# Kernel tuning notes

Measured on AMD Instinct MI355X. Metric: run time of the kernel, lower is better.

Reference implementation:

```python
import jax, jax.numpy as jnp
import numpy as np

N_LEVELS = 4
F_DIM = 2
B = 1_000_000
SIZES = [12 * ((2 ** (l - 1)) ** 2 + 2) for l in range(1, N_LEVELS + 1)]  # [36, 72, 216, 792]
MAX_SIZE = max(SIZES)  # 792
NPIX = [12 * (2 ** i) ** 2 for i in range(N_LEVELS)]  # [12, 48, 192, 768]


def setup_inputs() -> dict:
    key = jax.random.key(0)
    ks = jax.random.split(key, 6)
    # learned table, init uniform(-1e-4, 1e-4) as in the torch module
    params = jax.random.uniform(ks[0], (N_LEVELS, MAX_SIZE, F_DIM),
                                minval=-1e-4, maxval=1e-4, dtype=jnp.float32)
    # per-level HEALPix pixel indices, each in [0, npix_level)
    pixel_index = jnp.stack([
        jax.random.randint(jax.random.fold_in(ks[1], i), (B,), 0, NPIX[i], dtype=jnp.int32)
        for i in range(N_LEVELS)])
    neigh = jnp.stack([
        jax.random.randint(jax.random.fold_in(ks[2], i), (8, B), 0, NPIX[i], dtype=jnp.int32)
        for i in range(N_LEVELS)])
    drop = jax.random.uniform(ks[3], (N_LEVELS, 8, B)) < 0.05
    neigh_index = jnp.where(drop, jnp.int32(-1), neigh)
    # latlon in radians: theta in [0, pi], phi in [0, 2*pi)
    u_p = jax.random.uniform(ks[4], (N_LEVELS, B, 2))
    pixel_latlon = jnp.stack([u_p[..., 0] * jnp.pi, u_p[..., 1] * (2 * jnp.pi)], axis=-1).astype(jnp.float32)
    u_n = jax.random.uniform(ks[5], (N_LEVELS, 8 * B, 2))
    neigh_latlon = jnp.stack([u_n[..., 0] * jnp.pi, u_n[..., 1] * (2 * jnp.pi)], axis=-1).astype(jnp.float32)
    return {"params": params, "pixel_latlon": pixel_latlon, "neigh_latlon": neigh_latlon,
            "pixel_index": pixel_index, "neigh_index": neigh_index}


def reference(params, pixel_latlon, neigh_latlon, pixel_index, neigh_index):
    L, _, F = params.shape  # [L, max_size, F]
    Bp = pixel_index.shape[1]
    # index_preprocessing: -1 -> max(index)+1, build keep-mask
    nflat = neigh_index.reshape(L, -1)  # [L, 8B]
    miss = nflat == -1
    nflat = jnp.where(miss, nflat.max() + 1, nflat)
    nmask = (~miss).astype(params.dtype)  # [L, 8B]
    pidx = jnp.where(pixel_index == -1, pixel_index.max() + 1, pixel_index)  # [L, B]
    # gathers from the parameter table
    neigh_reps = jnp.take_along_axis(params, nflat[..., None], axis=1)   # [L, 8B, F]
    my_reps = jnp.take_along_axis(params, pidx[..., None], axis=1)       # [L, B, F]
    # inverse-distance weights (equirectangular "great circle" per source)
    my_ll = jnp.broadcast_to(pixel_latlon[:, None], (L, 8, Bp, 2)).reshape(L, 8 * Bp, 2)
    d = jnp.sqrt((neigh_latlon[..., 1] - my_ll[..., 1]) ** 2 +
                 (neigh_latlon[..., 0] - my_ll[..., 0]) ** 2)  # [L, 8B]
    d = jnp.where(jnp.isinf(d), d.min(), d)
    w = 1.0 / d
    # weight, mask, sum over 8 neighbors, add residual
    out = (neigh_reps * w[..., None]).reshape(L, 8, Bp, F) * nmask.reshape(L, 8, Bp)[..., None]
    out = out.sum(axis=1) + my_reps  # [L, B, F]
    # faithful to torch: reshape(4, -1).t().reshape(-1, L*F)
    out = out.reshape(4, -1).T.reshape(-1, L * F)
    return out.astype(jnp.float32)
```

## Files before the change

kernel.cpp:

```cpp
#include <hip/hip_runtime.h>


#define NLEV 4
#define MAXSZ 792
#define TABSZ (NLEV * MAXSZ * 2)
#define PPB 128
#define OSTRIDE 12

__global__ __launch_bounds__(512) void heal_encoding_kernel(
    const float* __restrict__ params,
    const float* __restrict__ pixel_latlon,
    const float* __restrict__ neigh_latlon,
    const int*   __restrict__ pixel_index,
    const int*   __restrict__ neigh_index,
    float* __restrict__ out,
    int B)
{
    __shared__ float stab[TABSZ];
    __shared__ float sout[PPB * OSTRIDE];

    const int tid = threadIdx.x;
    const int bl  = tid & (PPB - 1);
    const int l   = tid >> 7;
    const int b_raw = blockIdx.x * PPB + bl;
    const int b = min(b_raw, B - 1);

    const float2* pll2 = (const float2*)pixel_latlon;
    const float2* nll2 = (const float2*)neigh_latlon;

    int   pi  = pixel_index[l * B + b];
    float2 pll = pll2[l * B + b];
    int    ni[8];
    float2 nl[8];
    #pragma unroll
    for (int j = 0; j < 8; ++j) {
        ni[j] = neigh_index[(l * 8 + j) * B + b];
        nl[j] = nll2[(l * 8 + j) * B + b];
    }

    {
        const float4* p4  = (const float4*)params;
        float4*       st4 = (float4*)stab;
        for (int i = tid; i < TABSZ / 4; i += 512)
            st4[i] = p4[i];
    }
    __syncthreads();

    const float2* sp2 = (const float2*)stab;
    const int lbase = l * MAXSZ;

    float a0 = 0.0f, a1 = 0.0f;
    #pragma unroll
    for (int j = 0; j < 8; ++j) {
        float dth = nl[j].x - pll.x;
        float dph = nl[j].y - pll.y;
        float d   = sqrtf(dth * dth + dph * dph);
        float w   = (ni[j] >= 0) ? (1.0f / d) : 0.0f;
        float2 r  = sp2[lbase + (ni[j] >= 0 ? ni[j] : 0)];
        a0 += w * r.x;
        a1 += w * r.y;
    }
    float2 m = sp2[lbase + (pi < 0 ? 768 : pi)];
    a0 += m.x;
    a1 += m.y;

    sout[bl * OSTRIDE + l]     = a0;
    sout[bl * OSTRIDE + 4 + l] = a1;
    __syncthreads();

    if (tid < 2 * PPB) {
        int px = tid >> 1;
        int h  = tid & 1;
        int bo = blockIdx.x * PPB + px;
        if (bo < B) {
            float4 v = *(const float4*)&sout[px * OSTRIDE + 4 * h];
            ((float4*)(out + (size_t)bo * 8))[h] = v;
        }
    }
}

extern "C" void kernel_launch(void* const* d_in, const int* in_sizes, int n_in,
                              void* d_out, int out_size, void* d_ws, size_t ws_size,
                              hipStream_t stream) {
    const float* params       = (const float*)d_in[0];
    const float* pixel_latlon = (const float*)d_in[1];
    const float* neigh_latlon = (const float*)d_in[2];
    const int*   pixel_index  = (const int*)d_in[3];
    const int*   neigh_index  = (const int*)d_in[4];
    float* out = (float*)d_out;

    int B = in_sizes[3] / NLEV;
    int blocks = (B + PPB - 1) / PPB;
    heal_encoding_kernel<<<blocks, 512, 0, stream>>>(
        params, pixel_latlon, neigh_latlon, pixel_index, neigh_index, out, B);
}
```

Before: 457.9 us.

## Make kernel persistent, interleave levels per lane, write output via shuffle

Switches to a persistent grid-stride launch capped at 1536 blocks of 256 threads. Each block loads the shared parameter table once and reuses it across many 64-pixel tiles, instead of reloading it for every 128-pixel block. Threads are remapped so the four levels of a pixel sit in adjacent lanes. Output is then assembled with a lane shuffle and float2 stores, removing the shared-memory staging buffer and the second barrier. The trade-off is that global loads within a wavefront split into four 16-element segments, one per level, so they are less contiguous than before.

```diff
diff --git a/kernel.cpp b/kernel.cpp
--- a/kernel.cpp
+++ b/kernel.cpp
@@ -4,78 +4,74 @@
 #define NLEV 4
 #define MAXSZ 792
 #define TABSZ (NLEV * MAXSZ * 2)
-#define PPB 128
-#define OSTRIDE 12
+#define PPB 64
 
-__global__ __launch_bounds__(512) void heal_encoding_kernel(
+__global__ __launch_bounds__(256, 6) void heal_encoding_kernel(
     const float* __restrict__ params,
     const float* __restrict__ pixel_latlon,
     const float* __restrict__ neigh_latlon,
     const int*   __restrict__ pixel_index,
     const int*   __restrict__ neigh_index,
     float* __restrict__ out,
-    int B)
+    int B, int ntiles)
 {
     __shared__ float stab[TABSZ];
-    __shared__ float sout[PPB * OSTRIDE];
 
     const int tid = threadIdx.x;
-    const int bl  = tid & (PPB - 1);
-    const int l   = tid >> 7;
-    const int b_raw = blockIdx.x * PPB + bl;
-    const int b = min(b_raw, B - 1);
-
-    const float2* pll2 = (const float2*)pixel_latlon;
-    const float2* nll2 = (const float2*)neigh_latlon;
-
-    int   pi  = pixel_index[l * B + b];
-    float2 pll = pll2[l * B + b];
-    int    ni[8];
-    float2 nl[8];
-    #pragma unroll
-    for (int j = 0; j < 8; ++j) {
-        ni[j] = neigh_index[(l * 8 + j) * B + b];
-        nl[j] = nll2[(l * 8 + j) * B + b];
-    }
+    const int bl  = tid >> 2;
+    const int l   = tid & 3;
 
     {
         const float4* p4  = (const float4*)params;
         float4*       st4 = (float4*)stab;
-        for (int i = tid; i < TABSZ / 4; i += 512)
+        for (int i = tid; i < TABSZ / 4; i += 256)
             st4[i] = p4[i];
     }
     __syncthreads();
 
-    const float2* sp2 = (const float2*)stab;
-    const int lbase = l * MAXSZ;
+    const float2* sp2  = (const float2*)stab;
+    const float2* pll2 = (const float2*)pixel_latlon;
+    const float2* nll2 = (const float2*)neigh_latlon;
+    const int lb = l * MAXSZ;
+    const int pb = l * B;
+    const int nb = l * 8 * B;
 
-    float a0 = 0.0f, a1 = 0.0f;
-    #pragma unroll
-    for (int j = 0; j < 8; ++j) {
-        float dth = nl[j].x - pll.x;
-        float dph = nl[j].y - pll.y;
-        float d   = sqrtf(dth * dth + dph * dph);
-        float w   = (ni[j] >= 0) ? (1.0f / d) : 0.0f;
-        float2 r  = sp2[lbase + (ni[j] >= 0 ? ni[j] : 0)];
-        a0 += w * r.x;
-        a1 += w * r.y;
-    }
-    float2 m = sp2[lbase + (pi < 0 ? 768 : pi)];
-    a0 += m.x;
-    a1 += m.y;
+    for (int t = blockIdx.x; t < ntiles; t += gridDim.x) {
+        const int b_raw = t * PPB + bl;
+        const int b = min(b_raw, B - 1);
 
-    sout[bl * OSTRIDE + l]     = a0;
-    sout[bl * OSTRIDE + 4 + l] = a1;
-    __syncthreads();
+        const int    pi  = pixel_index[pb + b];
+        const float2 pll = pll2[pb + b];
+        int    ni[8];
+        float2 nl[8];
+        #pragma unroll
+        for (int j = 0; j < 8; ++j) {
+            ni[j] = neigh_index[nb + j * B + b];
+            nl[j] = nll2[nb + j * B + b];
+        }
 
-    if (tid < 2 * PPB) {
-        int px = tid >> 1;
-        int h  = tid & 1;
-        int bo = blockIdx.x * PPB + px;
-        if (bo < B) {
-            float4 v = *(const float4*)&sout[px * OSTRIDE + 4 * h];
-            ((float4*)(out + (size_t)bo * 8))[h] = v;
+        float a0 = 0.0f, a1 = 0.0f;
+        #pragma unroll
+        for (int j = 0; j < 8; ++j) {
+            float dth = nl[j].x - pll.x;
+            float dph = nl[j].y - pll.y;
+            float d   = sqrtf(dth * dth + dph * dph);
+            float w   = (ni[j] >= 0) ? (1.0f / d) : 0.0f;
+            float2 r  = sp2[lb + (ni[j] >= 0 ? ni[j] : 0)];
+            a0 += w * r.x;
+            a1 += w * r.y;
         }
+        float2 m = sp2[lb + (pi < 0 ? 768 : pi)];
+        a0 += m.x;
+        a1 += m.y;
+
+        const bool odd = (l & 1);
+        float x = __shfl_xor(odd ? a0 : a1, 1);
+        float2 st = odd ? make_float2(x, a1)
+                        : make_float2(a0, x);
+        const int col = odd ? (l + 3) : l;
+        if (b_raw < B)
+            *(float2*)(out + (size_t)b_raw * 8 + col) = st;
     }
 }
 
@@ -90,7 +86,9 @@
     float* out = (float*)d_out;
 
     int B = in_sizes[3] / NLEV;
-    int blocks = (B + PPB - 1) / PPB;
-    heal_encoding_kernel<<<blocks, 512, 0, stream>>>(
-        params, pixel_latlon, neigh_latlon, pixel_index, neigh_index, out, B);
+    int ntiles = (B + PPB - 1) / PPB;
+    int blocks = 1536;
+    if (blocks > ntiles) blocks = ntiles;
+    heal_encoding_kernel<<<blocks, 256, 0, stream>>>(
+        params, pixel_latlon, neigh_latlon, pixel_index, neigh_index, out, B, ntiles);
 }
```

Result: slower. 470.6 us (+2.8%).
